# Kernel optimization log

Measured on AMD Instinct MI355X. Metric: run time of the kernel, lower is better.

The kernel has to match this reference:

```python
import jax, jax.numpy as jnp
import numpy as np

B, N, D = 4096, 64, 256  # batch, n_nodes, d_input


def setup_inputs() -> dict:
    key = jax.random.key(0)
    k = jax.random.split(key, 6)
    return {
        "x": jax.random.normal(k[0], (B, N, D), dtype=jnp.float32),
        "W1": jax.random.normal(k[1], (1,), dtype=jnp.float32),
        "W2": jax.random.normal(k[2], (D, 1), dtype=jnp.float32),
        "W3": jax.random.normal(k[3], (D,), dtype=jnp.float32),
        "bs": jax.random.normal(k[4], (1, N, N), dtype=jnp.float32),
        "Vs": jax.random.normal(k[5], (N, N), dtype=jnp.float32),
    }


def reference(x, W1, W2, W3, bs, Vs):
    # x: (B, N, D). Dropout is identity (inference / p=0).
    # LHS = (x * W1) @ W2  -> (B, N, 1); collapse to (B, N)
    lhs = jnp.einsum("bnd,d->bn", x, W2[:, 0]) * W1[0]
    # RHS = W3 @ x (over feature dim) -> (B, N); used as (B, 1, N)
    rhs = jnp.einsum("bnd,d->bn", x, W3)
    # scores: Vs @ tanh(outer(lhs, rhs) + bs)  -> (B, N, N)
    t = jnp.tanh(lhs[:, :, None] * rhs[:, None, :] + bs)  # (B, N, N)
    s = jnp.einsum("ij,bjk->bik", Vs, t)  # (B, N, N)
    # softmax over the flattened N*N scores per batch element
    a = jax.nn.softmax(s.reshape(x.shape[0], -1), axis=-1)
    return a.reshape(-1, N, N)
```

## Files before the change

kernel.cpp:

```cpp
#include <hip/hip_runtime.h>


typedef float f32x4 __attribute__((ext_vector_type(4)));
typedef __bf16 bf16x8 __attribute__((ext_vector_type(8)));

__global__ __launch_bounds__(256, 4) void adjatt_kernel(
    const float* __restrict__ x,
    const float* __restrict__ W1,
    const float* __restrict__ W2,
    const float* __restrict__ W3,
    const float* __restrict__ bs,
    const float* __restrict__ Vs,
    float* __restrict__ out)
{
    __shared__ __align__(16) unsigned char tT[16384];
    __shared__ __align__(16) float lhs[64];
    __shared__ __align__(16) float rhs[64];
    __shared__ float redm[4], reds[4];

    const int tid  = threadIdx.x;
    const int b    = blockIdx.x;
    const int lane = tid & 63;
    const int w    = tid >> 6;

    const float W1v = W1[0];

    bf16x8 Ah[2], Al[2];
    {
        const int row = 16 * w + (lane & 15);
        #pragma unroll
        for (int s = 0; s < 2; ++s) {
            const float* vp = Vs + row * 64 + 32 * s + 8 * (lane >> 4);
            f32x4 f0 = *(const f32x4*)vp;
            f32x4 f1 = *(const f32x4*)(vp + 4);
            #pragma unroll
            for (int e = 0; e < 4; ++e) {
                __bf16 h0 = (__bf16)f0[e];
                Ah[s][e] = h0;
                Al[s][e] = (__bf16)(f0[e] - (float)h0);
                __bf16 h1 = (__bf16)f1[e];
                Ah[s][e + 4] = h1;
                Al[s][e + 4] = (__bf16)(f1[e] - (float)h1);
            }
        }
    }

    {
        const int co = tid & 15;
        const int r0 = tid >> 4;
        f32x4 w2v[4], w3v[4];
        #pragma unroll
        for (int kk = 0; kk < 4; ++kk) {
            w2v[kk] = *(const f32x4*)(W2 + 4 * (co + 16 * kk));
            w3v[kk] = *(const f32x4*)(W3 + 4 * (co + 16 * kk));
        }
        const float* xb = x + (size_t)b * 16384;
        #pragma unroll
        for (int it = 0; it < 4; ++it) {
            const int r = r0 + 16 * it;
            const float* xr = xb + r * 256;
            float d2 = 0.f, d3 = 0.f;
            #pragma unroll
            for (int kk = 0; kk < 4; ++kk) {
                f32x4 xv = *(const f32x4*)(xr + 4 * (co + 16 * kk));
                d2 = fmaf(xv[0], w2v[kk][0], d2); d2 = fmaf(xv[1], w2v[kk][1], d2);
                d2 = fmaf(xv[2], w2v[kk][2], d2); d2 = fmaf(xv[3], w2v[kk][3], d2);
                d3 = fmaf(xv[0], w3v[kk][0], d3); d3 = fmaf(xv[1], w3v[kk][1], d3);
                d3 = fmaf(xv[2], w3v[kk][2], d3); d3 = fmaf(xv[3], w3v[kk][3], d3);
            }
            d2 += __shfl_xor(d2, 1); d2 += __shfl_xor(d2, 2);
            d2 += __shfl_xor(d2, 4); d2 += __shfl_xor(d2, 8);
            d3 += __shfl_xor(d3, 1); d3 += __shfl_xor(d3, 2);
            d3 += __shfl_xor(d3, 4); d3 += __shfl_xor(d3, 8);
            if (co == 0) { lhs[r] = d2 * W1v; rhs[r] = d3; }
        }
    }
    __syncthreads();

    {
        const int n  = lane;
        const int j0 = 16 * w;
        const float rv = rhs[n];
        f32x4 lh[4];
        #pragma unroll
        for (int c = 0; c < 4; ++c) lh[c] = *(const f32x4*)&lhs[j0 + 4 * c];
        bf16x8 hi[2], lo[2];
        #pragma unroll
        for (int jj = 0; jj < 16; ++jj) {
            float z  = fmaf(lh[jj >> 2][jj & 3], rv, bs[(j0 + jj) * 64 + n]);
            float e2 = __expf(2.f * z);
            float th = 1.f - __fdividef(2.f, e2 + 1.f);
            __bf16 h = (__bf16)th;
            hi[jj >> 3][jj & 7] = h;
            lo[jj >> 3][jj & 7] = (__bf16)(th - (float)h);
        }
        #pragma unroll
        for (int c = 0; c < 2; ++c) {
            const int off = (n * 128 + (j0 + 8 * c) * 2) ^ ((n & 7) << 4);
            *(bf16x8*)(tT + off)        = hi[c];
            *(bf16x8*)(tT + 8192 + off) = lo[c];
        }
    }
    __syncthreads();

    f32x4 acc[4];
    #pragma unroll
    for (int nt = 0; nt < 4; ++nt) acc[nt] = (f32x4){0.f, 0.f, 0.f, 0.f};
    #pragma unroll
    for (int nt = 0; nt < 4; ++nt) {
        const int n = 16 * nt + (lane & 15);
        #pragma unroll
        for (int s = 0; s < 2; ++s) {
            const int off = (n * 128 + 64 * s + 16 * (lane >> 4)) ^ ((n & 7) << 4);
            bf16x8 Bh = *(const bf16x8*)(tT + off);
            bf16x8 Bl = *(const bf16x8*)(tT + 8192 + off);
            acc[nt] = __builtin_amdgcn_mfma_f32_16x16x32_bf16(Ah[s], Bh, acc[nt], 0, 0, 0);
            acc[nt] = __builtin_amdgcn_mfma_f32_16x16x32_bf16(Al[s], Bh, acc[nt], 0, 0, 0);
            acc[nt] = __builtin_amdgcn_mfma_f32_16x16x32_bf16(Ah[s], Bl, acc[nt], 0, 0, 0);
        }
    }

    float m = acc[0][0];
    #pragma unroll
    for (int nt = 0; nt < 4; ++nt)
        #pragma unroll
        for (int e = 0; e < 4; ++e) m = fmaxf(m, acc[nt][e]);
    #pragma unroll
    for (int off = 1; off < 64; off <<= 1) m = fmaxf(m, __shfl_xor(m, off));
    if (lane == 0) redm[w] = m;
    __syncthreads();
    const float M = fmaxf(fmaxf(redm[0], redm[1]), fmaxf(redm[2], redm[3]));

    float ssum = 0.f;
    #pragma unroll
    for (int nt = 0; nt < 4; ++nt)
        #pragma unroll
        for (int e = 0; e < 4; ++e) {
            acc[nt][e] = __expf(acc[nt][e] - M);
            ssum += acc[nt][e];
        }
    #pragma unroll
    for (int off = 1; off < 64; off <<= 1) ssum += __shfl_xor(ssum, off);
    if (lane == 0) reds[w] = ssum;
    __syncthreads();
    const float inv = __fdividef(1.f, reds[0] + reds[1] + reds[2] + reds[3]);

    float* ob = out + (size_t)b * 4096;
    const int rbase = 16 * w + 4 * (lane >> 4);
    const int cbase = lane & 15;
    #pragma unroll
    for (int nt = 0; nt < 4; ++nt) {
        const int col = 16 * nt + cbase;
        #pragma unroll
        for (int e = 0; e < 4; ++e) {
            ob[(rbase + e) * 64 + col] = acc[nt][e] * inv;
        }
    }
}

extern "C" void kernel_launch(void* const* d_in, const int* in_sizes, int n_in,
                              void* d_out, int out_size, void* d_ws, size_t ws_size,
                              hipStream_t stream) {
    const float* x  = (const float*)d_in[0];
    const float* W1 = (const float*)d_in[1];
    const float* W2 = (const float*)d_in[2];
    const float* W3 = (const float*)d_in[3];
    const float* bs = (const float*)d_in[4];
    const float* Vs = (const float*)d_in[5];
    float* out = (float*)d_out;

    const int B = in_sizes[0] / (64 * 256);
    adjatt_kernel<<<dim3(B), dim3(256), 0, stream>>>(x, W1, W2, W3, bs, Vs, out);
}
```

Baseline: 69.74 us.

## Swap MFMA operands for vector stores, single-pass online softmax, prefetch bs

Swaps the A and B operands of the MFMA so each lane's accumulator holds four consecutive columns of one output row. The result can then be written with 16-byte vector stores instead of scattered scalar stores. The softmax now uses per-wave max and sum combined through one shared exchange with rescaling, which removes one block-wide barrier. The bs values are also loaded into registers at kernel start to hide their latency, at the cost of 16 extra registers per thread and a few extra exp evaluations.

```diff
diff --git a/kernel.cpp b/kernel.cpp
--- a/kernel.cpp
+++ b/kernel.cpp
@@ -2,6 +2,7 @@
 
 
 typedef float f32x4 __attribute__((ext_vector_type(4)));
+typedef float f32x2 __attribute__((ext_vector_type(2)));
 typedef __bf16 bf16x8 __attribute__((ext_vector_type(8)));
 
 __global__ __launch_bounds__(256, 4) void adjatt_kernel(
@@ -16,31 +17,40 @@
     __shared__ __align__(16) unsigned char tT[16384];
     __shared__ __align__(16) float lhs[64];
     __shared__ __align__(16) float rhs[64];
-    __shared__ float redm[4], reds[4];
+    __shared__ f32x2 red[4];
 
     const int tid  = threadIdx.x;
     const int b    = blockIdx.x;
     const int lane = tid & 63;
     const int w    = tid >> 6;
+    const int l15  = lane & 15;
+    const int g    = lane >> 4;
 
     const float W1v = W1[0];
 
-    bf16x8 Ah[2], Al[2];
+    float bsv[16];
     {
-        const int row = 16 * w + (lane & 15);
+        const int j0 = 16 * w;
         #pragma unroll
-        for (int s = 0; s < 2; ++s) {
-            const float* vp = Vs + row * 64 + 32 * s + 8 * (lane >> 4);
+        for (int jj = 0; jj < 16; ++jj) bsv[jj] = bs[(j0 + jj) * 64 + lane];
+    }
+
+    bf16x8 Vh[2], Vl[2];
+    {
+        const int row = 16 * w + l15;
+        #pragma unroll
+        for (int sk = 0; sk < 2; ++sk) {
+            const float* vp = Vs + row * 64 + 32 * sk + 8 * g;
             f32x4 f0 = *(const f32x4*)vp;
             f32x4 f1 = *(const f32x4*)(vp + 4);
             #pragma unroll
             for (int e = 0; e < 4; ++e) {
                 __bf16 h0 = (__bf16)f0[e];
-                Ah[s][e] = h0;
-                Al[s][e] = (__bf16)(f0[e] - (float)h0);
+                Vh[sk][e] = h0;
+                Vl[sk][e] = (__bf16)(f0[e] - (float)h0);
                 __bf16 h1 = (__bf16)f1[e];
-                Ah[s][e + 4] = h1;
-                Al[s][e + 4] = (__bf16)(f1[e] - (float)h1);
+                Vh[sk][e + 4] = h1;
+                Vl[sk][e + 4] = (__bf16)(f1[e] - (float)h1);
             }
         }
     }
@@ -87,7 +97,7 @@
         bf16x8 hi[2], lo[2];
         #pragma unroll
         for (int jj = 0; jj < 16; ++jj) {
-            float z  = fmaf(lh[jj >> 2][jj & 3], rv, bs[(j0 + jj) * 64 + n]);
+            float z  = fmaf(lh[jj >> 2][jj & 3], rv, bsv[jj]);
             float e2 = __expf(2.f * z);
             float th = 1.f - __fdividef(2.f, e2 + 1.f);
             __bf16 h = (__bf16)th;
@@ -105,56 +115,51 @@
 
     f32x4 acc[4];
     #pragma unroll
-    for (int nt = 0; nt < 4; ++nt) acc[nt] = (f32x4){0.f, 0.f, 0.f, 0.f};
+    for (int ct = 0; ct < 4; ++ct) acc[ct] = (f32x4){0.f, 0.f, 0.f, 0.f};
     #pragma unroll
-    for (int nt = 0; nt < 4; ++nt) {
-        const int n = 16 * nt + (lane & 15);
+    for (int ct = 0; ct < 4; ++ct) {
+        const int n = 16 * ct + l15;
         #pragma unroll
-        for (int s = 0; s < 2; ++s) {
-            const int off = (n * 128 + 64 * s + 16 * (lane >> 4)) ^ ((n & 7) << 4);
-            bf16x8 Bh = *(const bf16x8*)(tT + off);
-            bf16x8 Bl = *(const bf16x8*)(tT + 8192 + off);
-            acc[nt] = __builtin_amdgcn_mfma_f32_16x16x32_bf16(Ah[s], Bh, acc[nt], 0, 0, 0);
-            acc[nt] = __builtin_amdgcn_mfma_f32_16x16x32_bf16(Al[s], Bh, acc[nt], 0, 0, 0);
-            acc[nt] = __builtin_amdgcn_mfma_f32_16x16x32_bf16(Ah[s], Bl, acc[nt], 0, 0, 0);
+        for (int sk = 0; sk < 2; ++sk) {
+            const int off = (n * 128 + 64 * sk + 16 * g) ^ ((n & 7) << 4);
+            bf16x8 Th = *(const bf16x8*)(tT + off);
+            bf16x8 Tl = *(const bf16x8*)(tT + 8192 + off);
+            acc[ct] = __builtin_amdgcn_mfma_f32_16x16x32_bf16(Th, Vh[sk], acc[ct], 0, 0, 0);
+            acc[ct] = __builtin_amdgcn_mfma_f32_16x16x32_bf16(Tl, Vh[sk], acc[ct], 0, 0, 0);
+            acc[ct] = __builtin_amdgcn_mfma_f32_16x16x32_bf16(Th, Vl[sk], acc[ct], 0, 0, 0);
         }
     }
 
     float m = acc[0][0];
     #pragma unroll
-    for (int nt = 0; nt < 4; ++nt)
+    for (int ct = 0; ct < 4; ++ct)
         #pragma unroll
-        for (int e = 0; e < 4; ++e) m = fmaxf(m, acc[nt][e]);
+        for (int e = 0; e < 4; ++e) m = fmaxf(m, acc[ct][e]);
     #pragma unroll
     for (int off = 1; off < 64; off <<= 1) m = fmaxf(m, __shfl_xor(m, off));
-    if (lane == 0) redm[w] = m;
-    __syncthreads();
-    const float M = fmaxf(fmaxf(redm[0], redm[1]), fmaxf(redm[2], redm[3]));
-
     float ssum = 0.f;
     #pragma unroll
-    for (int nt = 0; nt < 4; ++nt)
+    for (int ct = 0; ct < 4; ++ct)
         #pragma unroll
         for (int e = 0; e < 4; ++e) {
-            acc[nt][e] = __expf(acc[nt][e] - M);
-            ssum += acc[nt][e];
+            acc[ct][e] = __expf(acc[ct][e] - m);
+            ssum += acc[ct][e];
         }
     #pragma unroll
     for (int off = 1; off < 64; off <<= 1) ssum += __shfl_xor(ssum, off);
-    if (lane == 0) reds[w] = ssum;
+    if (lane == 0) red[w] = (f32x2){m, ssum};
     __syncthreads();
-    const float inv = __fdividef(1.f, reds[0] + reds[1] + reds[2] + reds[3]);
+    const f32x2 r0v = red[0], r1v = red[1], r2v = red[2], r3v = red[3];
+    const float M = fmaxf(fmaxf(r0v[0], r1v[0]), fmaxf(r2v[0], r3v[0]));
+    const float S = r0v[1] * __expf(r0v[0] - M) + r1v[1] * __expf(r1v[0] - M) +
+                    r2v[1] * __expf(r2v[0] - M) + r3v[1] * __expf(r3v[0] - M);
+    const float f = __expf(m - M) * __fdividef(1.f, S);
 
-    float* ob = out + (size_t)b * 4096;
-    const int rbase = 16 * w + 4 * (lane >> 4);
-    const int cbase = lane & 15;
+    float* ob = out + (size_t)b * 4096 + (16 * w + l15) * 64 + 4 * g;
     #pragma unroll
-    for (int nt = 0; nt < 4; ++nt) {
-        const int col = 16 * nt + cbase;
-        #pragma unroll
-        for (int e = 0; e < 4; ++e) {
-            ob[(rbase + e) * 64 + col] = acc[nt][e] * inv;
-        }
+    for (int ct = 0; ct < 4; ++ct) {
+        f32x4 v = {acc[ct][0] * f, acc[ct][1] * f, acc[ct][2] * f, acc[ct][3] * f};
+        *(f32x4*)(ob + 16 * ct) = v;
     }
 }
 
```

Result: no change. 68.92 us (-1.2%).
